# Optimization experiments

Measured on AMD Instinct MI355X. Metric: run time of the kernel, lower is better.

The kernel has to match this reference:

```python
import jax, jax.numpy as jnp
import numpy as np

# Static config (matches init_kwargs)
VOCAB, EMBED, HIDDEN = 32000, 256, 512
SLOTS, MEM_DIM, HEADS, TOPK = 1024, 64, 4, 8
B, T = 16, 128
# beta_read/beta_write are learned scalars but the torch forward detaches them
# via .item(); treat as constants (|beta| + 1e-6 with beta init ~1.0).
BETA_R = 1.0 + 1e-6
BETA_W = 1.0 + 1e-6
EPS = 1e-8


def setup_inputs() -> dict:
    key = jax.random.key(0)
    ks = jax.random.split(key, 16)
    s = 0.02
    HD = HEADS * MEM_DIM
    return {
        "input_seq": jax.random.randint(ks[0], (B, T), 0, VOCAB),
        "E": jax.random.normal(ks[1], (VOCAB, EMBED), jnp.float32) * s,
        "W_ih": jax.random.normal(ks[2], (4 * HIDDEN, EMBED + MEM_DIM), jnp.float32) * s,
        "W_hh": jax.random.normal(ks[3], (4 * HIDDEN, HIDDEN), jnp.float32) * s,
        "b_ih": jnp.zeros((4 * HIDDEN,), jnp.float32),
        "b_hh": jnp.zeros((4 * HIDDEN,), jnp.float32),
        "W_out": jax.random.normal(ks[4], (HIDDEN, VOCAB), jnp.float32) * s,
        "b_out": jnp.zeros((VOCAB,), jnp.float32),
        "W_rk": jax.random.normal(ks[5], (HIDDEN, HD), jnp.float32) * s,
        "b_rk": jnp.zeros((HD,), jnp.float32),
        "W_wk": jax.random.normal(ks[6], (HIDDEN, HD), jnp.float32) * s,
        "b_wk": jnp.zeros((HD,), jnp.float32),
        "W_wv": jax.random.normal(ks[7], (HIDDEN, HD), jnp.float32) * s,
        "b_wv": jnp.zeros((HD,), jnp.float32),
        "W_er": jax.random.normal(ks[8], (HIDDEN, HD), jnp.float32) * s,
        "b_er": jnp.zeros((HD,), jnp.float32),
    }


def _address(memory, keys, beta):
    # memory: [B,S,D], keys: [B,H,D] -> sparse (top-k) content weights [B,H,S]
    mem_n = memory / (jnp.linalg.norm(memory, axis=-1, keepdims=True) + EPS)
    key_n = keys / (jnp.linalg.norm(keys, axis=-1, keepdims=True) + EPS)
    scores = beta * jnp.einsum("bhd,bsd->bhs", key_n, mem_n)
    vals, idx = jax.lax.top_k(scores, TOPK)           # [B,H,K]
    sm = jax.nn.softmax(vals, axis=-1)                # softmax over top-k only
    w = jnp.zeros_like(scores)
    b_ix = jnp.arange(scores.shape[0])[:, None, None]
    h_ix = jnp.arange(HEADS)[None, :, None]
    return w.at[b_ix, h_ix, idx].set(sm)              # [B,H,S]


def reference(input_seq, E, W_ih, W_hh, b_ih, b_hh, W_out, b_out,
              W_rk, b_rk, W_wk, b_wk, W_wv, b_wv, W_er, b_er):
    Bq = input_seq.shape[0]
    memory0 = jnp.full((Bq, SLOTS, MEM_DIM), 1e-6, jnp.float32)
    h0 = jnp.zeros((Bq, HIDDEN), jnp.float32)
    c0 = jnp.zeros((Bq, HIDDEN), jnp.float32)
    r0 = jnp.zeros((Bq, MEM_DIM), jnp.float32)

    def step(carry, x_t):
        memory, h, c, read_vec = carry
        emb = E[x_t]                                          # [B,embed]
        inp = jnp.concatenate([emb, read_vec], axis=-1)
        gates = inp @ W_ih.T + b_ih + h @ W_hh.T + b_hh       # [B,4H]
        i, f, g, o = jnp.split(gates, 4, axis=-1)             # torch LSTM order
        c = jax.nn.sigmoid(f) * c + jax.nn.sigmoid(i) * jnp.tanh(g)
        h = jax.nn.sigmoid(o) * jnp.tanh(c)
        logits = h @ W_out + b_out                            # [B,V]
        rk = (h @ W_rk + b_rk).reshape(Bq, HEADS, MEM_DIM)
        wk = (h @ W_wk + b_wk).reshape(Bq, HEADS, MEM_DIM)
        wv = (h @ W_wv + b_wv).reshape(Bq, HEADS, MEM_DIM)
        er = jax.nn.sigmoid(h @ W_er + b_er).reshape(Bq, HEADS, MEM_DIM)
        # content-addressed top-k read
        rw = _address(memory, rk, BETA_R)                     # [B,H,S]
        read_vec = jnp.einsum("bhs,bsd->bhd", rw, memory).mean(axis=1)
        # erase + add write
        ww = _address(memory, wk, BETA_W)                     # [B,H,S]
        keep = jnp.prod(1.0 - ww[..., None] * er[:, :, None, :], axis=1)
        add = jnp.einsum("bhs,bhd->bsd", ww, wv)
        memory = memory * keep + add
        return (memory, h, c, read_vec), logits

    _, logits_seq = jax.lax.scan(step, (memory0, h0, c0, r0), input_seq.T)
    return jnp.transpose(logits_seq, (1, 0, 2))               # [B,T,V]
```

## Files before the change

### kernel.cpp

```cpp
#include <hip/hip_runtime.h>
#include <hip/hip_bf16.h>
#include <stdint.h>

typedef unsigned int uint;
typedef unsigned long long u64;

#define T_STEPS 128
#define BQ 16
#define HID 512
#define NSLOT 1024
#define MD 64
#define VOCAB 32000
#define NWG 128
#define BETA 1.000001f
#define EPSN 1e-8f

#define L_MEM  0
#define L_NRM  8704
#define L_WS   8832
#define L_HS   12960
#define L_KEY  21216
#define L_KNRM 21728
#define L_SC   21736
#define L_WV   22760
#define L_ER   23016
#define L_WL   23272
#define L_GL   23336
#define L_RV   23592
#define L_TOT  24616

#define AL4(dst, p) asm volatile("global_load_dwordx4 %0, %1, off sc0 sc1" : "=v"(dst) : "v"(p))
#define ALF(dst, p) asm volatile("global_load_dword %0, %1, off sc0 sc1" : "=v"(dst) : "v"(p))
#define AWAIT() do { asm volatile("s_waitcnt vmcnt(0)" ::: "memory"); __builtin_amdgcn_sched_barrier(0); } while(0)

__device__ __forceinline__ float sigm(float x){ return 1.f/(1.f+expf(-x)); }
__device__ __forceinline__ void astoref(float* p, float v){
  __hip_atomic_store(p, v, __ATOMIC_RELAXED, __HIP_MEMORY_SCOPE_AGENT);
}
__device__ __forceinline__ void astoreu64(u64* p, u64 v){
  __hip_atomic_store(p, v, __ATOMIC_RELAXED, __HIP_MEMORY_SCOPE_AGENT);
}
__device__ __forceinline__ u64 aloadu64(const u64* p){
  return __hip_atomic_load((u64*)p, __ATOMIC_RELAXED, __HIP_MEMORY_SCOPE_AGENT);
}
__device__ __forceinline__ uint aloadu32(const uint* p){
  return __hip_atomic_load((uint*)p, __ATOMIC_RELAXED, __HIP_MEMORY_SCOPE_AGENT);
}

__device__ __forceinline__ u64 packsc(float v, int slot){
  uint u = __float_as_uint(v);
  u = (u & 0x80000000u) ? ~u : (u | 0x80000000u);
  return ((u64)u << 10) | (u64)(1023 - slot);
}
__device__ __forceinline__ float unpackval(u64 p){
  uint u = (uint)(p >> 10);
  uint bits = (u & 0x80000000u) ? (u & 0x7fffffffu) : ~u;
  return __uint_as_float(bits);
}
__device__ __forceinline__ int unpackslot(u64 p){ return 1023 - (int)(p & 1023u); }

__device__ __forceinline__ void b_arrive(uint* arrv, uint gen){
  asm volatile("s_waitcnt vmcnt(0)" ::: "memory");
  __syncthreads();
  if (threadIdx.x == 0)
    __hip_atomic_store(arrv + (size_t)blockIdx.x*32, gen, __ATOMIC_RELAXED, __HIP_MEMORY_SCOPE_AGENT);
}
__device__ __forceinline__ void b_wait(uint* arrv, uint gen){
  if (blockIdx.x == 0){
    if (threadIdx.x < NWG){
      while (aloadu32(arrv + (size_t)threadIdx.x*32) < gen)
        __builtin_amdgcn_s_sleep(1);
    }
    __syncthreads();
    if (threadIdx.x < 16)
      __hip_atomic_store(arrv + (size_t)(NWG + threadIdx.x)*32, gen, __ATOMIC_RELAXED, __HIP_MEMORY_SCOPE_AGENT);
    __syncthreads();
  } else {
    if (threadIdx.x == 0){
      while (aloadu32(arrv + (size_t)(NWG + (blockIdx.x & 15))*32) < gen)
        __builtin_amdgcn_s_sleep(1);
    }
    __syncthreads();
  }
}

__global__ __launch_bounds__(256) void prep_emb(const float* __restrict__ E,
                                                const int* __restrict__ seq,
                                                float* __restrict__ EMB){
  int m = blockIdx.x;
  int t = m >> 4, b = m & 15;
  int x = seq[b*T_STEPS + t];
  EMB[(size_t)m*256 + threadIdx.x] = E[(size_t)x*256 + threadIdx.x];
}

__global__ __launch_bounds__(256) void gemm_emb(const float* __restrict__ A,
                                                const float* __restrict__ W_ih,
                                                const float* __restrict__ b_ih,
                                                const float* __restrict__ b_hh,
                                                float* __restrict__ C){
  __shared__ __align__(16) float As[16*68];
  __shared__ __align__(16) float Bs[16*68];
  int mt = blockIdx.x & 31, nt = blockIdx.x >> 5;
  int m0 = mt*64, n0 = nt*64;
  int tx = threadIdx.x & 15, ty = threadIdx.x >> 4;
  float acc[4][4] = {};
  for (int k0 = 0; k0 < 256; k0 += 16){
    int mm = threadIdx.x >> 2, kq = (threadIdx.x & 3)*4;
    float4 a = *(const float4*)(A + (size_t)(m0+mm)*256 + k0 + kq);
    As[(kq+0)*68+mm]=a.x; As[(kq+1)*68+mm]=a.y; As[(kq+2)*68+mm]=a.z; As[(kq+3)*68+mm]=a.w;
    int pp = n0 + mm;
    int r = (pp & 3)*512 + (pp >> 2);
    float4 bv = *(const float4*)(W_ih + (size_t)r*320 + k0 + kq);
    Bs[(kq+0)*68+mm]=bv.x; Bs[(kq+1)*68+mm]=bv.y; Bs[(kq+2)*68+mm]=bv.z; Bs[(kq+3)*68+mm]=bv.w;
    __syncthreads();
    #pragma unroll
    for (int kk = 0; kk < 16; ++kk){
      float4 av = *(const float4*)(As + kk*68 + ty*4);
      float4 bb = *(const float4*)(Bs + kk*68 + tx*4);
      float aa[4] = {av.x,av.y,av.z,av.w};
      float bv2[4] = {bb.x,bb.y,bb.z,bb.w};
      #pragma unroll
      for (int i = 0; i < 4; ++i)
        #pragma unroll
        for (int j = 0; j < 4; ++j)
          acc[i][j] = fmaf(aa[i], bv2[j], acc[i][j]);
    }
    __syncthreads();
  }
  #pragma unroll
  for (int i = 0; i < 4; ++i){
    int m = m0 + ty*4 + i;
    #pragma unroll
    for (int j = 0; j < 4; ++j){
      int pp = n0 + tx*4 + j;
      int r = (pp & 3)*512 + (pp >> 2);
      C[(size_t)m*2048 + pp] = acc[i][j] + b_ih[r] + b_hh[r];
    }
  }
}

__global__ __launch_bounds__(256, 1) void recurrent_kernel(
    const float* __restrict__ W_hh, const float* __restrict__ W_ih,
    const float* __restrict__ W_rk, const float* __restrict__ b_rk,
    const float* __restrict__ W_wk, const float* __restrict__ b_wk,
    const float* __restrict__ W_wv, const float* __restrict__ b_wv,
    const float* __restrict__ W_er, const float* __restrict__ b_er,
    const float* __restrict__ G_emb, float* __restrict__ H_all,
    float* __restrict__ mem_g, float* __restrict__ projbuf,
    float* __restrict__ rv_g, u64* __restrict__ cand,
    u64* __restrict__ wlist, uint* __restrict__ arrv)
{
  __shared__ __align__(16) float smem[L_TOT];
  float* mem_s  = smem + L_MEM;
  float* nrm_s  = smem + L_NRM;
  float* Ws     = smem + L_WS;
  float* hs     = smem + L_HS;
  float* key_s  = smem + L_KEY;
  float* knrm_s = smem + L_KNRM;
  float* sc_s   = smem + L_SC;
  float* wv_s   = smem + L_WV;
  float* er_s   = smem + L_ER;
  u64*   wl_s   = (u64*)(smem + L_WL);
  float* gl     = smem + L_GL;
  float* rv_st  = smem + L_RV;

  const int tid = threadIdx.x;
  const int wg  = blockIdx.x;
  float c_reg = 0.f;

  const int p1_b = tid >> 4, p1_col = tid & 15;
  const int pcol = wg*16 + p1_col;
  const int rrow = (pcol & 3)*512 + (pcol >> 2);
  const int msel = wg >> 5;
  const int col0 = (wg & 31)*8;
  const float* Wm  = (msel==0)? W_rk : (msel==1)? W_wk : (msel==2)? W_wv : W_er;
  const float* bmp = (msel==0)? b_rk : (msel==1)? b_wk : (msel==2)? b_wv : b_er;
  const int bb3 = wg >> 3, rg = wg & 7, s0 = rg*128;
  float* mslice_g = mem_g + ((size_t)bb3*NSLOT + s0)*MD;

  for (int i = tid; i < 8*HID; i += 256){
    int k = i >> 3, j = i & 7;
    Ws[j*516 + k] = Wm[(size_t)k*256 + col0 + j];
  }
  for (int i = tid; i < 128*MD; i += 256){
    mem_s[(i >> 6)*68 + (i & 63)] = 1e-6f;
    astoref(mslice_g + i, 1e-6f);
  }
  gl[p1_b*16 + p1_col] = G_emb[(size_t)p1_b*2048 + pcol];
  __syncthreads();
  if (p1_col < 4){
    float gi = gl[p1_b*16 + p1_col*4 + 0];
    float gf = gl[p1_b*16 + p1_col*4 + 1];
    float gg = gl[p1_b*16 + p1_col*4 + 2];
    float go = gl[p1_b*16 + p1_col*4 + 3];
    c_reg = sigm(gf)*c_reg + sigm(gi)*tanhf(gg);
    float h = sigm(go)*tanhf(c_reg);
    astoref(H_all + (size_t)p1_b*HID + wg*4 + p1_col, h);
  }
  b_arrive(arrv, 1);

  #pragma clang loop unroll(disable)
  for (int t = 0; t < T_STEPS-1; ++t){
    const uint g0 = (uint)(4*t);
    b_wait(arrv, g0 + 1);

    {
      const float4* hsrc = (const float4*)(H_all + (size_t)t*BQ*HID);
      for (int i = tid; i < BQ*HID/4; i += 256){
        int b = i >> 7, q = i & 127;
        *(float4*)(hs + b*516 + q*4) = hsrc[i];
      }
      __syncthreads();
      int b = tid >> 4, o2 = (tid & 15) >> 1, half = tid & 1;
      const float4* wp = (const float4*)(Ws + o2*516 + half*256);
      const float4* xp = (const float4*)(hs + b*516 + half*256);
      float a0 = 0.f, a1 = 0.f;
      #pragma unroll 4
      for (int k = 0; k < 64; k += 2){
        float4 w = wp[k], x = xp[k];
        a0=fmaf(w.x,x.x,a0); a0=fmaf(w.y,x.y,a0); a0=fmaf(w.z,x.z,a0); a0=fmaf(w.w,x.w,a0);
        w = wp[k+1]; x = xp[k+1];
        a1=fmaf(w.x,x.x,a1); a1=fmaf(w.y,x.y,a1); a1=fmaf(w.z,x.z,a1); a1=fmaf(w.w,x.w,a1);
      }
      float acc = a0 + a1;
      float other = __shfl_xor(acc, 1);
      if (half == 0){
        float v = acc + other + bmp[col0 + o2];
        if (msel == 3) v = sigm(v);
        astoref(projbuf + (size_t)(t&1)*BQ*1024 + (size_t)b*1024 + msel*256 + col0 + o2, v);
      }
    }
    b_arrive(arrv, g0 + 2);

    float gp;
    {
      const int parp = (t & 1) ^ 1;
      if (t > 0){
        const float* projp = projbuf + (size_t)parp*BQ*1024 + (size_t)bb3*1024;
        if (tid < 32)
          wl_s[tid] = aloadu64(wlist + (size_t)bb3*32 + tid);
        if (tid < 64){
          float4 v; AL4(v, (const float4*)(projp + 512) + tid); AWAIT();
          *(float4*)(wv_s + tid*4) = v;
        } else if (tid < 128){
          int i = tid - 64;
          float4 v; AL4(v, (const float4*)(projp + 768) + i); AWAIT();
          *(float4*)(er_s + i*4) = v;
        }
      }
      __syncthreads();
      if (t > 0 && tid < 64){
        const int d = tid;
        #pragma unroll 1
        for (int e = 0; e < 32; ++e){
          u64 w64 = wl_s[e];
          int sl = (int)(w64 & 0xffffffffu);
          if (sl >= s0 && sl < s0+128){
            float w = __uint_as_float((uint)(w64 >> 32));
            mem_s[(sl-s0)*68 + d] *= (1.f - w*er_s[(e >> 3)*64 + d]);
          }
        }
        #pragma unroll 1
        for (int e = 0; e < 32; ++e){
          u64 w64 = wl_s[e];
          int sl = (int)(w64 & 0xffffffffu);
          if (sl >= s0 && sl < s0+128){
            float w = __uint_as_float((uint)(w64 >> 32));
            mem_s[(sl-s0)*68 + d] += w*wv_s[(e >> 3)*64 + d];
          }
        }
        #pragma unroll 1
        for (int e = 0; e < 32; ++e){
          u64 w64 = wl_s[e];
          int sl = (int)(w64 & 0xffffffffu);
          if (sl >= s0 && sl < s0+128)
            astoref(mslice_g + (sl-s0)*MD + d, mem_s[(sl-s0)*68 + d]);
        }
      }
      __syncthreads();
      {
        int s = tid >> 1, half = tid & 1;
        const float4* mp = (const float4*)(mem_s + s*68 + half*32);
        float sum = 0.f;
        #pragma unroll
        for (int q = 0; q < 8; ++q){
          float4 v = mp[q];
          sum = fmaf(v.x,v.x,sum); sum = fmaf(v.y,v.y,sum);
          sum = fmaf(v.z,v.z,sum); sum = fmaf(v.w,v.w,sum);
        }
        sum += __shfl_xor(sum, 1);
        if (half == 0) nrm_s[s] = sqrtf(sum) + EPSN;
      }
      {
        float a0 = G_emb[(size_t)((t+1)*BQ + p1_b)*2048 + pcol];
        float a1 = 0.f, a2 = 0.f, a3 = 0.f;
        const float4* wh = (const float4*)(W_hh + (size_t)rrow*HID);
        const float4* xv = (const float4*)(hs + p1_b*516);
        #pragma unroll 2
        for (int k = 0; k < 128; k += 4){
          float4 w, x;
          w=wh[k+0]; x=xv[k+0]; a0=fmaf(w.x,x.x,a0); a0=fmaf(w.y,x.y,a0); a0=fmaf(w.z,x.z,a0); a0=fmaf(w.w,x.w,a0);
          w=wh[k+1]; x=xv[k+1]; a1=fmaf(w.x,x.x,a1); a1=fmaf(w.y,x.y,a1); a1=fmaf(w.z,x.z,a1); a1=fmaf(w.w,x.w,a1);
          w=wh[k+2]; x=xv[k+2]; a2=fmaf(w.x,x.x,a2); a2=fmaf(w.y,x.y,a2); a2=fmaf(w.z,x.z,a2); a2=fmaf(w.w,x.w,a2);
          w=wh[k+3]; x=xv[k+3]; a3=fmaf(w.x,x.x,a3); a3=fmaf(w.y,x.y,a3); a3=fmaf(w.w,x.w,a3); a3=fmaf(w.z,x.z,a3);
        }
        gp = (a0+a1)+(a2+a3);
      }
    }
    b_wait(arrv, g0 + 2);

    {
      const float* projb = projbuf + (size_t)(t&1)*BQ*1024 + (size_t)bb3*1024;
      if (tid < 128){
        float4 kv; AL4(kv, (const float4*)projb + tid); AWAIT();
        *(float4*)(key_s + tid*4) = kv;
      }
      __syncthreads();
      if (tid < 8){
        const float4* kp = (const float4*)(key_s + tid*MD);
        float sum = 0.f;
        #pragma unroll
        for (int q = 0; q < 16; ++q){
          float4 v = kp[q];
          sum = fmaf(v.x,v.x,sum); sum = fmaf(v.y,v.y,sum);
          sum = fmaf(v.z,v.z,sum); sum = fmaf(v.w,v.w,sum);
        }
        knrm_s[tid] = sqrtf(sum) + EPSN;
      }
      __syncthreads();
      {
        int s = tid >> 1, kh = tid & 1;
        const float4* mp = (const float4*)(mem_s + s*68);
        float rnm = 1.f / nrm_s[s];
        float acc4[4] = {0.f,0.f,0.f,0.f};
        #pragma unroll
        for (int q = 0; q < 16; ++q){
          float4 m = mp[q];
          #pragma unroll
          for (int kk = 0; kk < 4; ++kk){
            float4 k4 = *(const float4*)(key_s + (kh*4+kk)*MD + q*4);
            acc4[kk] = fmaf(m.x,k4.x,acc4[kk]); acc4[kk] = fmaf(m.y,k4.y,acc4[kk]);
            acc4[kk] = fmaf(m.z,k4.z,acc4[kk]); acc4[kk] = fmaf(m.w,k4.w,acc4[kk]);
          }
        }
        #pragma unroll
        for (int kk = 0; kk < 4; ++kk){
          int key = kh*4 + kk;
          sc_s[key*128 + s] = BETA * acc4[kk] * rnm / knrm_s[key];
        }
      }
      __syncthreads();
      {
        int wid = tid >> 6, lane = tid & 63;
        #pragma unroll
        for (int kk = 0; kk < 2; ++kk){
          int key = wid*2 + kk;
          u64 p0 = packsc(sc_s[key*128 + lane],      s0 + lane);
          u64 p1 = packsc(sc_s[key*128 + 64 + lane], s0 + 64 + lane);
          #pragma unroll
          for (int r = 0; r < 8; ++r){
            u64 m = p0 > p1 ? p0 : p1;
            #pragma unroll
            for (int o = 32; o; o >>= 1){ u64 q = __shfl_xor(m, o); if (q > m) m = q; }
            if (p0 == m) p0 = 0; else if (p1 == m) p1 = 0;
            if (lane == 0) astoreu64(cand + (((size_t)bb3*8 + key)*8 + rg)*8 + r, m);
          }
        }
      }
    }
    b_arrive(arrv, g0 + 3);
    b_wait(arrv, g0 + 3);

    if (wg < BQ){
      const int bb = wg;
      int wid = tid >> 6, lane = tid & 63;
      #pragma unroll
      for (int kk = 0; kk < 2; ++kk){
        int key = wid*2 + kk;
        u64 pv = aloadu64(cand + (((size_t)bb*8 + key)*8 + (lane >> 3))*8 + (lane & 7));
        u64 sel = 0;
        #pragma unroll
        for (int r = 0; r < 8; ++r){
          u64 m = pv;
          #pragma unroll
          for (int o = 32; o; o >>= 1){ u64 q = __shfl_xor(m, o); if (q > m) m = q; }
          if (pv == m) pv = 0;
          if (lane == r) sel = m;
        }
        float val = unpackval(sel);
        int slot = unpackslot(sel);
        float vmax = __shfl(val, 0);
        float e = (lane < 8) ? expf(val - vmax) : 0.f;
        float ssum = e;
        #pragma unroll
        for (int o = 32; o; o >>= 1) ssum += __shfl_xor(ssum, o);
        float w = e / ssum;
        if (key < 4){
          int sls[8];
          #pragma unroll
          for (int i = 0; i < 8; ++i) sls[i] = __shfl(slot, i);
          float mv[8];
          #pragma unroll
          for (int i = 0; i < 8; ++i)
            ALF(mv[i], mem_g + ((size_t)bb*NSLOT + sls[i])*MD + lane);
          AWAIT();
          float acc = 0.f;
          #pragma unroll
          for (int i = 0; i < 8; ++i) acc = fmaf(__shfl(w, i), mv[i], acc);
          rv_st[key*64 + lane] = acc;
        } else if (lane < 8){
          astoreu64(wlist + (size_t)bb*32 + (key-4)*8 + lane,
                    ((u64)__float_as_uint(w) << 32) | (u64)(uint)slot);
        }
      }
      __syncthreads();
      if (tid < 64){
        float m = 0.25f*(rv_st[tid] + rv_st[64+tid] + rv_st[128+tid] + rv_st[192+tid]);
        astoref(rv_g + (size_t)bb*MD + tid, m);
      }
    }
    b_arrive(arrv, g0 + 4);
    b_wait(arrv, g0 + 4);

    {
      float4 rvv; AL4(rvv, (const float4*)rv_g + tid); AWAIT();
      *(float4*)(rv_st + tid*4) = rvv;
      __syncthreads();
      float a0 = gp, a1 = 0.f;
      const float4* wi = (const float4*)(W_ih + (size_t)rrow*320 + 256);
      const float4* xr = (const float4*)(rv_st + p1_b*64);
      #pragma unroll
      for (int k = 0; k < 16; k += 2){
        float4 w = wi[k], x = xr[k];
        a0=fmaf(w.x,x.x,a0); a0=fmaf(w.y,x.y,a0); a0=fmaf(w.z,x.z,a0); a0=fmaf(w.w,x.w,a0);
        w = wi[k+1]; x = xr[k+1];
        a1=fmaf(w.x,x.x,a1); a1=fmaf(w.y,x.y,a1); a1=fmaf(w.z,x.z,a1); a1=fmaf(w.w,x.w,a1);
      }
      gl[p1_b*16 + p1_col] = a0 + a1;
      __syncthreads();
      if (p1_col < 4){
        float gi = gl[p1_b*16 + p1_col*4 + 0];
        float gf = gl[p1_b*16 + p1_col*4 + 1];
        float gg = gl[p1_b*16 + p1_col*4 + 2];
        float go = gl[p1_b*16 + p1_col*4 + 3];
        c_reg = sigm(gf)*c_reg + sigm(gi)*tanhf(gg);
        float h = sigm(go)*tanhf(c_reg);
        astoref(H_all + (size_t)((t+1)*BQ + p1_b)*HID + wg*4 + p1_col, h);
      }
    }
    b_arrive(arrv, g0 + 5);
  }
}

__global__ __launch_bounds__(256) void gemm_out(const float* __restrict__ A,
                                                const float* __restrict__ Bmat,
                                                const float* __restrict__ bias,
                                                float* __restrict__ C){
  __shared__ __align__(16) float As[16*132];
  __shared__ __align__(16) float Bs[16*64];
  int mt = blockIdx.x & 15, nt = blockIdx.x >> 4;
  int m0 = mt*128, n0 = nt*64;
  int tx = threadIdx.x & 15, ty = threadIdx.x >> 4;
  float acc[8][4] = {};
  for (int k0 = 0; k0 < 512; k0 += 16){
    int mm = threadIdx.x >> 1, kq = (threadIdx.x & 1)*8;
    float4 a0 = *(const float4*)(A + (size_t)(m0+mm)*512 + k0 + kq);
    float4 a1 = *(const float4*)(A + (size_t)(m0+mm)*512 + k0 + kq + 4);
    As[(kq+0)*132+mm]=a0.x; As[(kq+1)*132+mm]=a0.y; As[(kq+2)*132+mm]=a0.z; As[(kq+3)*132+mm]=a0.w;
    As[(kq+4)*132+mm]=a1.x; As[(kq+5)*132+mm]=a1.y; As[(kq+6)*132+mm]=a1.z; As[(kq+7)*132+mm]=a1.w;
    int kk2 = threadIdx.x >> 4, nq = (threadIdx.x & 15)*4;
    *(float4*)(Bs + kk2*64 + nq) = *(const float4*)(Bmat + (size_t)(k0+kk2)*VOCAB + n0 + nq);
    __syncthreads();
    #pragma unroll
    for (int kk = 0; kk < 16; ++kk){
      float4 x0 = *(const float4*)(As + kk*132 + ty*8);
      float4 x1 = *(const float4*)(As + kk*132 + ty*8 + 4);
      float4 bv = *(const float4*)(Bs + kk*64 + tx*4);
      float aa[8] = {x0.x,x0.y,x0.z,x0.w,x1.x,x1.y,x1.z,x1.w};
      float bb[4] = {bv.x,bv.y,bv.z,bv.w};
      #pragma unroll
      for (int i = 0; i < 8; ++i)
        #pragma unroll
        for (int j = 0; j < 4; ++j)
          acc[i][j] = fmaf(aa[i], bb[j], acc[i][j]);
    }
    __syncthreads();
  }
  #pragma unroll
  for (int i = 0; i < 8; ++i){
    int m = m0 + ty*8 + i;
    int bq = m & 15, tt = m >> 4;
    float* crow = C + ((size_t)bq*T_STEPS + tt)*VOCAB + n0 + tx*4;
    #pragma unroll
    for (int j = 0; j < 4; ++j) crow[j] = acc[i][j] + bias[n0 + tx*4 + j];
  }
}

extern "C" void kernel_launch(void* const* d_in, const int* in_sizes, int n_in,
                              void* d_out, int out_size, void* d_ws, size_t ws_size,
                              hipStream_t stream){
  const int*   seq   = (const int*)d_in[0];
  const float* E     = (const float*)d_in[1];
  const float* W_ih  = (const float*)d_in[2];
  const float* W_hh  = (const float*)d_in[3];
  const float* b_ih  = (const float*)d_in[4];
  const float* b_hh  = (const float*)d_in[5];
  const float* W_out = (const float*)d_in[6];
  const float* b_out = (const float*)d_in[7];
  const float* W_rk  = (const float*)d_in[8];
  const float* b_rk  = (const float*)d_in[9];
  const float* W_wk  = (const float*)d_in[10];
  const float* b_wk  = (const float*)d_in[11];
  const float* W_wv  = (const float*)d_in[12];
  const float* b_wv  = (const float*)d_in[13];
  const float* W_er  = (const float*)d_in[14];
  const float* b_er  = (const float*)d_in[15];
  float* out = (float*)d_out;
  (void)in_sizes; (void)n_in; (void)out_size; (void)ws_size;

  char* ws = (char*)d_ws;
  size_t off = 0;
  auto alloc = [&](size_t bytes) -> void* {
    off = (off + 255) & ~(size_t)255;
    void* p = ws + off;
    off += bytes;
    return p;
  };
  float* EMB     = (float*)alloc((size_t)2048*256*4);
  float* G_emb   = (float*)alloc((size_t)2048*2048*4);
  float* H_all   = (float*)alloc((size_t)2048*512*4);
  float* memb    = (float*)alloc((size_t)16*1024*64*4);
  float* projbuf = (float*)alloc((size_t)2*16*1024*4);
  float* rv_g    = (float*)alloc((size_t)16*64*4);
  u64*   cand    = (u64*)alloc((size_t)16*8*8*8*8);
  u64*   wlist   = (u64*)alloc((size_t)16*32*8);
  uint*  arrv    = (uint*)alloc((size_t)(NWG+16)*32*4);

  hipMemsetAsync(arrv, 0, (size_t)(NWG+16)*32*4, stream);
  prep_emb<<<2048, 256, 0, stream>>>(E, seq, EMB);
  gemm_emb<<<1024, 256, 0, stream>>>(EMB, W_ih, b_ih, b_hh, G_emb);
  recurrent_kernel<<<NWG, 256, 0, stream>>>(W_hh, W_ih, W_rk, b_rk, W_wk, b_wk,
                                            W_wv, b_wv, W_er, b_er,
                                            G_emb, H_all, memb, projbuf, rv_g,
                                            cand, wlist, arrv);
  gemm_out<<<16*500, 256, 0, stream>>>(H_all, W_out, b_out, out);
}
```

Measured before the change: 7.368 ms.

## Replace global barriers with point-to-point flags and dedicated per-batch LSTM workgroups

Replaces the centralized grid barrier (workgroup 0 gathers arrivals and rebroadcasts) with fine-grained per-producer flag lines that consumers poll directly. Adds 16 dedicated workgroups, one per batch row, that run top-k selection, the read vector and the LSTM cell update, while 128 workers handle memory slices, projections (now done by only 32 workgroups reading weights from global) and partial gate dot products. The read-vector part of W_ih is pre-transposed into a smem-resident tile. The goal is to cut barrier latency on the serial critical path per timestep, at the cost of more polling traffic and a more complex dependency chain.

```diff
diff --git a/kernel.cpp b/kernel.cpp
--- a/kernel.cpp
+++ b/kernel.cpp
@@ -11,32 +11,31 @@
 #define NSLOT 1024
 #define MD 64
 #define VOCAB 32000
-#define NWG 128
 #define BETA 1.000001f
 #define EPSN 1e-8f
 
-#define L_MEM  0
-#define L_NRM  8704
-#define L_WS   8832
-#define L_HS   12960
-#define L_KEY  21216
-#define L_KNRM 21728
-#define L_SC   21736
-#define L_WV   22760
-#define L_ER   23016
-#define L_WL   23272
-#define L_GL   23336
-#define L_RV   23592
-#define L_TOT  24616
+#define NWK 128
+#define NBT 16
+
+#define LF_FH(b)  ((b)*32)
+#define LF_FP(w)  ((16+(w))*32)
+#define LF_FC(w)  ((48+(w))*32)
+#define LF_FRV(b) ((176+(b))*32)
+#define LF_FG(w)  ((192+(w))*32)
+#define NLINES    320
 
 #define AL4(dst, p) asm volatile("global_load_dwordx4 %0, %1, off sc0 sc1" : "=v"(dst) : "v"(p))
 #define ALF(dst, p) asm volatile("global_load_dword %0, %1, off sc0 sc1" : "=v"(dst) : "v"(p))
 #define AWAIT() do { asm volatile("s_waitcnt vmcnt(0)" ::: "memory"); __builtin_amdgcn_sched_barrier(0); } while(0)
+#define DRAIN() asm volatile("s_waitcnt vmcnt(0)" ::: "memory")
 
 __device__ __forceinline__ float sigm(float x){ return 1.f/(1.f+expf(-x)); }
 __device__ __forceinline__ void astoref(float* p, float v){
   __hip_atomic_store(p, v, __ATOMIC_RELAXED, __HIP_MEMORY_SCOPE_AGENT);
 }
+__device__ __forceinline__ void astoreu32(uint* p, uint v){
+  __hip_atomic_store(p, v, __ATOMIC_RELAXED, __HIP_MEMORY_SCOPE_AGENT);
+}
 __device__ __forceinline__ void astoreu64(u64* p, u64 v){
   __hip_atomic_store(p, v, __ATOMIC_RELAXED, __HIP_MEMORY_SCOPE_AGENT);
 }
@@ -45,6 +44,9 @@
 }
 __device__ __forceinline__ uint aloadu32(const uint* p){
   return __hip_atomic_load((uint*)p, __ATOMIC_RELAXED, __HIP_MEMORY_SCOPE_AGENT);
+}
+__device__ __forceinline__ void poll1(const uint* p, uint gen){
+  while (aloadu32(p) < gen) __builtin_amdgcn_s_sleep(2);
 }
 
 __device__ __forceinline__ u64 packsc(float v, int slot){
@@ -59,36 +61,23 @@
 }
 __device__ __forceinline__ int unpackslot(u64 p){ return 1023 - (int)(p & 1023u); }
 
-__device__ __forceinline__ void b_arrive(uint* arrv, uint gen){
-  asm volatile("s_waitcnt vmcnt(0)" ::: "memory");
-  __syncthreads();
-  if (threadIdx.x == 0)
-    __hip_atomic_store(arrv + (size_t)blockIdx.x*32, gen, __ATOMIC_RELAXED, __HIP_MEMORY_SCOPE_AGENT);
-}
-__device__ __forceinline__ void b_wait(uint* arrv, uint gen){
-  if (blockIdx.x == 0){
-    if (threadIdx.x < NWG){
-      while (aloadu32(arrv + (size_t)threadIdx.x*32) < gen)
-        __builtin_amdgcn_s_sleep(1);
-    }
-    __syncthreads();
-    if (threadIdx.x < 16)
-      __hip_atomic_store(arrv + (size_t)(NWG + threadIdx.x)*32, gen, __ATOMIC_RELAXED, __HIP_MEMORY_SCOPE_AGENT);
-    __syncthreads();
-  } else {
-    if (threadIdx.x == 0){
-      while (aloadu32(arrv + (size_t)(NWG + (blockIdx.x & 15))*32) < gen)
-        __builtin_amdgcn_s_sleep(1);
-    }
-    __syncthreads();
-  }
-}
+#define L_MEM  0
+#define L_NRM  8704
+#define L_HS   8832
+#define L_KEY  17088
+#define L_KNRM 17600
+#define L_SC   17608
+#define L_WV   18632
+#define L_ER   18888
+#define L_WL   19144
+#define L_RVS  19208
+#define L_WTS  20232
+#define L_TOT  21256
 
 __global__ __launch_bounds__(256) void prep_emb(const float* __restrict__ E,
                                                 const int* __restrict__ seq,
                                                 float* __restrict__ EMB){
-  int m = blockIdx.x;
-  int t = m >> 4, b = m & 15;
+  int m = blockIdx.x, t = m >> 4, b = m & 15;
   int x = seq[b*T_STEPS + t];
   EMB[(size_t)m*256 + threadIdx.x] = E[(size_t)x*256 + threadIdx.x];
 }
@@ -139,180 +128,187 @@
   }
 }
 
-__global__ __launch_bounds__(256, 1) void recurrent_kernel(
-    const float* __restrict__ W_hh, const float* __restrict__ W_ih,
+__global__ __launch_bounds__(256) void make_wrvT(const float* __restrict__ W_ih,
+                                                 float* __restrict__ WT){
+  int idx = blockIdx.x*256 + threadIdx.x;
+  int k = idx >> 11, p = idx & 2047;
+  int r = (p & 3)*512 + (p >> 2);
+  WT[idx] = W_ih[(size_t)r*320 + 256 + k];
+}
+
+__global__ __launch_bounds__(256) void recur_kernel(
+    const float* __restrict__ W_hh, const float* __restrict__ WT,
     const float* __restrict__ W_rk, const float* __restrict__ b_rk,
     const float* __restrict__ W_wk, const float* __restrict__ b_wk,
     const float* __restrict__ W_wv, const float* __restrict__ b_wv,
     const float* __restrict__ W_er, const float* __restrict__ b_er,
     const float* __restrict__ G_emb, float* __restrict__ H_all,
-    float* __restrict__ mem_g, float* __restrict__ projbuf,
-    float* __restrict__ rv_g, u64* __restrict__ cand,
+    float* __restrict__ H_pub, float* __restrict__ mem_g,
+    float* __restrict__ projpub, float* __restrict__ gatespub,
+    float* __restrict__ rvpub, u64* __restrict__ cand,
     u64* __restrict__ wlist, uint* __restrict__ arrv)
 {
   __shared__ __align__(16) float smem[L_TOT];
-  float* mem_s  = smem + L_MEM;
-  float* nrm_s  = smem + L_NRM;
-  float* Ws     = smem + L_WS;
-  float* hs     = smem + L_HS;
-  float* key_s  = smem + L_KEY;
-  float* knrm_s = smem + L_KNRM;
-  float* sc_s   = smem + L_SC;
-  float* wv_s   = smem + L_WV;
-  float* er_s   = smem + L_ER;
-  u64*   wl_s   = (u64*)(smem + L_WL);
-  float* gl     = smem + L_GL;
-  float* rv_st  = smem + L_RV;
-
   const int tid = threadIdx.x;
   const int wg  = blockIdx.x;
-  float c_reg = 0.f;
-
-  const int p1_b = tid >> 4, p1_col = tid & 15;
-  const int pcol = wg*16 + p1_col;
-  const int rrow = (pcol & 3)*512 + (pcol >> 2);
-  const int msel = wg >> 5;
-  const int col0 = (wg & 31)*8;
-  const float* Wm  = (msel==0)? W_rk : (msel==1)? W_wk : (msel==2)? W_wv : W_er;
-  const float* bmp = (msel==0)? b_rk : (msel==1)? b_wk : (msel==2)? b_wv : b_er;
-  const int bb3 = wg >> 3, rg = wg & 7, s0 = rg*128;
-  float* mslice_g = mem_g + ((size_t)bb3*NSLOT + s0)*MD;
-
-  for (int i = tid; i < 8*HID; i += 256){
-    int k = i >> 3, j = i & 7;
-    Ws[j*516 + k] = Wm[(size_t)k*256 + col0 + j];
-  }
-  for (int i = tid; i < 128*MD; i += 256){
-    mem_s[(i >> 6)*68 + (i & 63)] = 1e-6f;
-    astoref(mslice_g + i, 1e-6f);
-  }
-  gl[p1_b*16 + p1_col] = G_emb[(size_t)p1_b*2048 + pcol];
-  __syncthreads();
-  if (p1_col < 4){
-    float gi = gl[p1_b*16 + p1_col*4 + 0];
-    float gf = gl[p1_b*16 + p1_col*4 + 1];
-    float gg = gl[p1_b*16 + p1_col*4 + 2];
-    float go = gl[p1_b*16 + p1_col*4 + 3];
-    c_reg = sigm(gf)*c_reg + sigm(gi)*tanhf(gg);
-    float h = sigm(go)*tanhf(c_reg);
-    astoref(H_all + (size_t)p1_b*HID + wg*4 + p1_col, h);
-  }
-  b_arrive(arrv, 1);
-
-  #pragma clang loop unroll(disable)
-  for (int t = 0; t < T_STEPS-1; ++t){
-    const uint g0 = (uint)(4*t);
-    b_wait(arrv, g0 + 1);
-
+
+  if (wg < NWK){
+    float* mem_s  = smem + L_MEM;
+    float* nrm_s  = smem + L_NRM;
+    float* hs     = smem + L_HS;
+    float* key_s  = smem + L_KEY;
+    float* knrm_s = smem + L_KNRM;
+    float* sc_s   = smem + L_SC;
+    float* wv_s   = smem + L_WV;
+    float* er_s   = smem + L_ER;
+    u64*   wl_s   = (u64*)(smem + L_WL);
+    float* rv_s   = smem + L_RVS;
+    float* WT_s   = smem + L_WTS;
+
+    const int b_s = wg >> 3, rg = wg & 7, s0 = rg*128;
+    const int gb = tid >> 4, gc = tid & 15;
+    const int pcol = wg*16 + gc;
+    const int rrow = (pcol & 3)*512 + (pcol >> 2);
+    float* mslice_g = mem_g + ((size_t)b_s*NSLOT + s0)*MD;
+    const float* W1 = (wg < 16) ? W_rk : W_wk;
+    const float* B1 = (wg < 16) ? b_rk : b_wk;
+    const float* W2 = (wg < 16) ? W_wv : W_er;
+    const float* B2 = (wg < 16) ? b_wv : b_er;
+    const int cc = (wg & 15)*16 + gc;
+    const float pb1 = (wg < 32) ? B1[cc] : 0.f;
+    const float pb2 = (wg < 32) ? B2[cc] : 0.f;
+
+    for (int i = tid; i < 64*16; i += 256){
+      int d = i >> 4, c = i & 15;
+      WT_s[i] = WT[(size_t)d*2048 + wg*16 + c];
+    }
+    for (int i = tid; i < 128*MD; i += 256){
+      mem_s[(i >> 6)*68 + (i & 63)] = 1e-6f;
+      astoref(mslice_g + i, 1e-6f);
+    }
+    __syncthreads();
     {
-      const float4* hsrc = (const float4*)(H_all + (size_t)t*BQ*HID);
-      for (int i = tid; i < BQ*HID/4; i += 256){
-        int b = i >> 7, q = i & 127;
-        *(float4*)(hs + b*516 + q*4) = hsrc[i];
-      }
-      __syncthreads();
-      int b = tid >> 4, o2 = (tid & 15) >> 1, half = tid & 1;
-      const float4* wp = (const float4*)(Ws + o2*516 + half*256);
-      const float4* xp = (const float4*)(hs + b*516 + half*256);
-      float a0 = 0.f, a1 = 0.f;
-      #pragma unroll 4
-      for (int k = 0; k < 64; k += 2){
-        float4 w = wp[k], x = xp[k];
-        a0=fmaf(w.x,x.x,a0); a0=fmaf(w.y,x.y,a0); a0=fmaf(w.z,x.z,a0); a0=fmaf(w.w,x.w,a0);
-        w = wp[k+1]; x = xp[k+1];
-        a1=fmaf(w.x,x.x,a1); a1=fmaf(w.y,x.y,a1); a1=fmaf(w.z,x.z,a1); a1=fmaf(w.w,x.w,a1);
-      }
-      float acc = a0 + a1;
-      float other = __shfl_xor(acc, 1);
-      if (half == 0){
-        float v = acc + other + bmp[col0 + o2];
-        if (msel == 3) v = sigm(v);
-        astoref(projbuf + (size_t)(t&1)*BQ*1024 + (size_t)b*1024 + msel*256 + col0 + o2, v);
-      }
-    }
-    b_arrive(arrv, g0 + 2);
-
-    float gp;
-    {
-      const int parp = (t & 1) ^ 1;
+      int s = tid >> 1, half = tid & 1;
+      const float4* mp = (const float4*)(mem_s + s*68 + half*32);
+      float sum = 0.f;
+      #pragma unroll
+      for (int q = 0; q < 8; ++q){
+        float4 v = mp[q];
+        sum = fmaf(v.x,v.x,sum); sum = fmaf(v.y,v.y,sum);
+        sum = fmaf(v.z,v.z,sum); sum = fmaf(v.w,v.w,sum);
+      }
+      sum += __shfl_xor(sum, 1);
+      if (half == 0) nrm_s[s] = sqrtf(sum) + EPSN;
+    }
+    __syncthreads();
+
+    #pragma clang loop unroll(disable)
+    for (int t = 0; t < T_STEPS-1; ++t){
+      const int par = t & 1, parp = par ^ 1;
       if (t > 0){
-        const float* projp = projbuf + (size_t)parp*BQ*1024 + (size_t)bb3*1024;
-        if (tid < 32)
-          wl_s[tid] = aloadu64(wlist + (size_t)bb3*32 + tid);
+        if (tid < 32) wl_s[tid] = aloadu64(wlist + (size_t)b_s*32 + tid);
         if (tid < 64){
-          float4 v; AL4(v, (const float4*)(projp + 512) + tid); AWAIT();
+          float4 v; AL4(v, (const float4*)(projpub + (size_t)parp*BQ*1024 + (size_t)b_s*1024 + 512) + tid);
+          AWAIT();
           *(float4*)(wv_s + tid*4) = v;
         } else if (tid < 128){
           int i = tid - 64;
-          float4 v; AL4(v, (const float4*)(projp + 768) + i); AWAIT();
+          float4 v; AL4(v, (const float4*)(projpub + (size_t)parp*BQ*1024 + (size_t)b_s*1024 + 768) + i);
+          AWAIT();
           *(float4*)(er_s + i*4) = v;
         }
-      }
-      __syncthreads();
-      if (t > 0 && tid < 64){
-        const int d = tid;
-        #pragma unroll 1
-        for (int e = 0; e < 32; ++e){
-          u64 w64 = wl_s[e];
-          int sl = (int)(w64 & 0xffffffffu);
-          if (sl >= s0 && sl < s0+128){
-            float w = __uint_as_float((uint)(w64 >> 32));
-            mem_s[(sl-s0)*68 + d] *= (1.f - w*er_s[(e >> 3)*64 + d]);
-          }
-        }
-        #pragma unroll 1
-        for (int e = 0; e < 32; ++e){
-          u64 w64 = wl_s[e];
-          int sl = (int)(w64 & 0xffffffffu);
-          if (sl >= s0 && sl < s0+128){
-            float w = __uint_as_float((uint)(w64 >> 32));
-            mem_s[(sl-s0)*68 + d] += w*wv_s[(e >> 3)*64 + d];
-          }
-        }
-        #pragma unroll 1
-        for (int e = 0; e < 32; ++e){
-          u64 w64 = wl_s[e];
-          int sl = (int)(w64 & 0xffffffffu);
-          if (sl >= s0 && sl < s0+128)
-            astoref(mslice_g + (sl-s0)*MD + d, mem_s[(sl-s0)*68 + d]);
-        }
-      }
-      __syncthreads();
-      {
-        int s = tid >> 1, half = tid & 1;
-        const float4* mp = (const float4*)(mem_s + s*68 + half*32);
-        float sum = 0.f;
-        #pragma unroll
-        for (int q = 0; q < 8; ++q){
-          float4 v = mp[q];
-          sum = fmaf(v.x,v.x,sum); sum = fmaf(v.y,v.y,sum);
-          sum = fmaf(v.z,v.z,sum); sum = fmaf(v.w,v.w,sum);
-        }
-        sum += __shfl_xor(sum, 1);
-        if (half == 0) nrm_s[s] = sqrtf(sum) + EPSN;
-      }
-      {
-        float a0 = G_emb[(size_t)((t+1)*BQ + p1_b)*2048 + pcol];
-        float a1 = 0.f, a2 = 0.f, a3 = 0.f;
-        const float4* wh = (const float4*)(W_hh + (size_t)rrow*HID);
-        const float4* xv = (const float4*)(hs + p1_b*516);
-        #pragma unroll 2
-        for (int k = 0; k < 128; k += 4){
-          float4 w, x;
-          w=wh[k+0]; x=xv[k+0]; a0=fmaf(w.x,x.x,a0); a0=fmaf(w.y,x.y,a0); a0=fmaf(w.z,x.z,a0); a0=fmaf(w.w,x.w,a0);
-          w=wh[k+1]; x=xv[k+1]; a1=fmaf(w.x,x.x,a1); a1=fmaf(w.y,x.y,a1); a1=fmaf(w.z,x.z,a1); a1=fmaf(w.w,x.w,a1);
-          w=wh[k+2]; x=xv[k+2]; a2=fmaf(w.x,x.x,a2); a2=fmaf(w.y,x.y,a2); a2=fmaf(w.z,x.z,a2); a2=fmaf(w.w,x.w,a2);
-          w=wh[k+3]; x=xv[k+3]; a3=fmaf(w.x,x.x,a3); a3=fmaf(w.y,x.y,a3); a3=fmaf(w.w,x.w,a3); a3=fmaf(w.z,x.z,a3);
-        }
-        gp = (a0+a1)+(a2+a3);
-      }
-    }
-    b_wait(arrv, g0 + 2);
-
-    {
-      const float* projb = projbuf + (size_t)(t&1)*BQ*1024 + (size_t)bb3*1024;
+        __syncthreads();
+        if (tid < 64){
+          const int d = tid;
+          #pragma unroll 1
+          for (int e = 0; e < 32; ++e){
+            u64 w64 = wl_s[e];
+            int sl = (int)(w64 & 0xffffffffu);
+            if (sl >= s0 && sl < s0+128){
+              float w = __uint_as_float((uint)(w64 >> 32));
+              mem_s[(sl-s0)*68 + d] *= (1.f - w*er_s[(e >> 3)*64 + d]);
+            }
+          }
+          #pragma unroll 1
+          for (int e = 0; e < 32; ++e){
+            u64 w64 = wl_s[e];
+            int sl = (int)(w64 & 0xffffffffu);
+            if (sl >= s0 && sl < s0+128){
+              float w = __uint_as_float((uint)(w64 >> 32));
+              mem_s[(sl-s0)*68 + d] += w*wv_s[(e >> 3)*64 + d];
+            }
+          }
+          #pragma unroll 1
+          for (int e = 0; e < 32; ++e){
+            u64 w64 = wl_s[e];
+            int sl = (int)(w64 & 0xffffffffu);
+            if (sl >= s0 && sl < s0+128)
+              astoref(mslice_g + (sl-s0)*MD + d, mem_s[(sl-s0)*68 + d]);
+          }
+        }
+        __syncthreads();
+        {
+          int s = tid >> 1, half = tid & 1;
+          const float4* mp = (const float4*)(mem_s + s*68 + half*32);
+          float sum = 0.f;
+          #pragma unroll
+          for (int q = 0; q < 8; ++q){
+            float4 v = mp[q];
+            sum = fmaf(v.x,v.x,sum); sum = fmaf(v.y,v.y,sum);
+            sum = fmaf(v.z,v.z,sum); sum = fmaf(v.w,v.w,sum);
+          }
+          sum += __shfl_xor(sum, 1);
+          if (half == 0) nrm_s[s] = sqrtf(sum) + EPSN;
+        }
+      }
+      if (tid < 16) poll1(arrv + LF_FH(tid), (uint)(t+1));
+      __syncthreads();
+      {
+        float4 v0,v1,v2,v3,v4,v5,v6,v7;
+        const float4* hp = (const float4*)H_pub;
+        AL4(v0, hp + tid);        AL4(v1, hp + tid + 256);
+        AL4(v2, hp + tid + 512);  AL4(v3, hp + tid + 768);
+        AL4(v4, hp + tid + 1024); AL4(v5, hp + tid + 1280);
+        AL4(v6, hp + tid + 1536); AL4(v7, hp + tid + 1792);
+        AWAIT();
+        int i;
+        i = tid;        *(float4*)(hs + (i>>7)*516 + (i&127)*4) = v0;
+        i = tid + 256;  *(float4*)(hs + (i>>7)*516 + (i&127)*4) = v1;
+        i = tid + 512;  *(float4*)(hs + (i>>7)*516 + (i&127)*4) = v2;
+        i = tid + 768;  *(float4*)(hs + (i>>7)*516 + (i&127)*4) = v3;
+        i = tid + 1024; *(float4*)(hs + (i>>7)*516 + (i&127)*4) = v4;
+        i = tid + 1280; *(float4*)(hs + (i>>7)*516 + (i&127)*4) = v5;
+        i = tid + 1536; *(float4*)(hs + (i>>7)*516 + (i&127)*4) = v6;
+        i = tid + 1792; *(float4*)(hs + (i>>7)*516 + (i&127)*4) = v7;
+      }
+      __syncthreads();
+      if (wg < 32){
+        float a0=0.f,a1=0.f,b0=0.f,b1=0.f;
+        const float* hp = hs + gb*516;
+        const float* w1 = W1 + cc;
+        const float* w2 = W2 + cc;
+        #pragma unroll 4
+        for (int k = 0; k < 512; k += 2){
+          float h0 = hp[k], h1 = hp[k+1];
+          a0 = fmaf(h0, w1[(size_t)k*256], a0);
+          b0 = fmaf(h0, w2[(size_t)k*256], b0);
+          a1 = fmaf(h1, w1[(size_t)(k+1)*256], a1);
+          b1 = fmaf(h1, w2[(size_t)(k+1)*256], b1);
+        }
+        float v1 = a0 + a1 + pb1;
+        float v2 = b0 + b1 + pb2;
+        if (wg >= 16) v2 = sigm(v2);
+        astoref(projpub + (size_t)par*BQ*1024 + (size_t)gb*1024 + wg*16 + gc, v1);
+        astoref(projpub + (size_t)par*BQ*1024 + (size_t)gb*1024 + 512 + wg*16 + gc, v2);
+      }
+      DRAIN();
+      __syncthreads();
+      if (wg < 32 && tid == 0) astoreu32(arrv + LF_FP(wg), (uint)(t+1));
+      if (tid < 32) poll1(arrv + LF_FP(tid), (uint)(t+1));
+      __syncthreads();
       if (tid < 128){
-        float4 kv; AL4(kv, (const float4*)projb + tid); AWAIT();
+        float4 kv; AL4(kv, (const float4*)(projpub + (size_t)par*BQ*1024 + (size_t)b_s*1024) + tid);
+        AWAIT();
         *(float4*)(key_s + tid*4) = kv;
       }
       __syncthreads();
@@ -363,92 +359,141 @@
             #pragma unroll
             for (int o = 32; o; o >>= 1){ u64 q = __shfl_xor(m, o); if (q > m) m = q; }
             if (p0 == m) p0 = 0; else if (p1 == m) p1 = 0;
-            if (lane == 0) astoreu64(cand + (((size_t)bb3*8 + key)*8 + rg)*8 + r, m);
-          }
-        }
-      }
-    }
-    b_arrive(arrv, g0 + 3);
-    b_wait(arrv, g0 + 3);
-
-    if (wg < BQ){
-      const int bb = wg;
-      int wid = tid >> 6, lane = tid & 63;
-      #pragma unroll
-      for (int kk = 0; kk < 2; ++kk){
-        int key = wid*2 + kk;
-        u64 pv = aloadu64(cand + (((size_t)bb*8 + key)*8 + (lane >> 3))*8 + (lane & 7));
-        u64 sel = 0;
-        #pragma unroll
-        for (int r = 0; r < 8; ++r){
-          u64 m = pv;
+            if (lane == 0) astoreu64(cand + (((size_t)b_s*8 + key)*8 + rg)*8 + r, m);
+          }
+        }
+      }
+      DRAIN();
+      __syncthreads();
+      if (tid == 0) astoreu32(arrv + LF_FC(wg), (uint)(t+1));
+      float gpv;
+      {
+        float a0 = G_emb[(size_t)((t+1)*BQ + gb)*2048 + pcol];
+        float a1 = 0.f, a2 = 0.f, a3 = 0.f;
+        const float4* wh = (const float4*)(W_hh + (size_t)rrow*HID);
+        const float4* xv = (const float4*)(hs + gb*516);
+        #pragma unroll 2
+        for (int k = 0; k < 128; k += 4){
+          float4 w, x;
+          w=wh[k+0]; x=xv[k+0]; a0=fmaf(w.x,x.x,a0); a0=fmaf(w.y,x.y,a0); a0=fmaf(w.z,x.z,a0); a0=fmaf(w.w,x.w,a0);
+          w=wh[k+1]; x=xv[k+1]; a1=fmaf(w.x,x.x,a1); a1=fmaf(w.y,x.y,a1); a1=fmaf(w.z,x.z,a1); a1=fmaf(w.w,x.w,a1);
+          w=wh[k+2]; x=xv[k+2]; a2=fmaf(w.x,x.x,a2); a2=fmaf(w.y,x.y,a2); a2=fmaf(w.z,x.z,a2); a2=fmaf(w.w,x.w,a2);
+          w=wh[k+3]; x=xv[k+3]; a3=fmaf(w.x,x.x,a3); a3=fmaf(w.y,x.y,a3); a3=fmaf(w.z,x.z,a3); a3=fmaf(w.w,x.w,a3);
+        }
+        gpv = (a0+a1)+(a2+a3);
+      }
+      if (tid < 16) poll1(arrv + LF_FRV(tid), (uint)(t+1));
+      __syncthreads();
+      {
+        float4 v; AL4(v, (const float4*)rvpub + tid); AWAIT();
+        *(float4*)(rv_s + tid*4) = v;
+      }
+      __syncthreads();
+      {
+        float acc = gpv;
+        #pragma unroll 8
+        for (int d = 0; d < 64; ++d)
+          acc = fmaf(rv_s[gb*64 + d], WT_s[d*16 + gc], acc);
+        astoref(gatespub + (size_t)gb*2048 + pcol, acc);
+      }
+      DRAIN();
+      __syncthreads();
+      if (tid == 0) astoreu32(arrv + LF_FG(wg), (uint)(t+1));
+    }
+  } else {
+    const int b = wg - NWK;
+    float* rv_st = smem;
+    float c0, c1;
+    {
+      float4 gA = *(const float4*)(G_emb + (size_t)b*2048 + tid*8);
+      float4 gB = *(const float4*)(G_emb + (size_t)b*2048 + tid*8 + 4);
+      c0 = sigm(gA.x)*tanhf(gA.z);
+      float h0v = sigm(gA.w)*tanhf(c0);
+      c1 = sigm(gB.x)*tanhf(gB.z);
+      float h1v = sigm(gB.w)*tanhf(c1);
+      astoref(H_pub + (size_t)b*HID + tid*2,     h0v);
+      astoref(H_pub + (size_t)b*HID + tid*2 + 1, h1v);
+      H_all[(size_t)b*HID + tid*2]     = h0v;
+      H_all[(size_t)b*HID + tid*2 + 1] = h1v;
+    }
+    DRAIN();
+    __syncthreads();
+    if (tid == 0) astoreu32(arrv + LF_FH(b), 1u);
+
+    #pragma clang loop unroll(disable)
+    for (int t = 0; t < T_STEPS-1; ++t){
+      if (tid < 8) poll1(arrv + LF_FC(b*8 + tid), (uint)(t+1));
+      __syncthreads();
+      {
+        int wid = tid >> 6, lane = tid & 63;
+        #pragma unroll
+        for (int kk = 0; kk < 2; ++kk){
+          int key = wid*2 + kk;
+          u64 pv = aloadu64(cand + (((size_t)b*8 + key)*8 + (lane >> 3))*8 + (lane & 7));
+          u64 sel = 0;
           #pragma unroll
-          for (int o = 32; o; o >>= 1){ u64 q = __shfl_xor(m, o); if (q > m) m = q; }
-          if (pv == m) pv = 0;
-          if (lane == r) sel = m;
-        }
-        float val = unpackval(sel);
-        int slot = unpackslot(sel);
-        float vmax = __shfl(val, 0);
-        float e = (lane < 8) ? expf(val - vmax) : 0.f;
-        float ssum = e;
-        #pragma unroll
-        for (int o = 32; o; o >>= 1) ssum += __shfl_xor(ssum, o);
-        float w = e / ssum;
-        if (key < 4){
-          int sls[8];
+          for (int r = 0; r < 8; ++r){
+            u64 m = pv;
+            #pragma unroll
+            for (int o = 32; o; o >>= 1){ u64 q = __shfl_xor(m, o); if (q > m) m = q; }
+            if (pv == m) pv = 0;
+            if (lane == r) sel = m;
+          }
+          float val = unpackval(sel);
+          int slot = unpackslot(sel);
+          float vmax = __shfl(val, 0);
+          float e = (lane < 8) ? expf(val - vmax) : 0.f;
+          float ssum = e;
           #pragma unroll
-          for (int i = 0; i < 8; ++i) sls[i] = __shfl(slot, i);
-          float mv[8];
-          #pragma unroll
-          for (int i = 0; i < 8; ++i)
-            ALF(mv[i], mem_g + ((size_t)bb*NSLOT + sls[i])*MD + lane);
-          AWAIT();
-          float acc = 0.f;
-          #pragma unroll
-          for (int i = 0; i < 8; ++i) acc = fmaf(__shfl(w, i), mv[i], acc);
-          rv_st[key*64 + lane] = acc;
-        } else if (lane < 8){
-          astoreu64(wlist + (size_t)bb*32 + (key-4)*8 + lane,
-                    ((u64)__float_as_uint(w) << 32) | (u64)(uint)slot);
+          for (int o = 32; o; o >>= 1) ssum += __shfl_xor(ssum, o);
+          float w = e / ssum;
+          if (key < 4){
+            int sls[8];
+            #pragma unroll
+            for (int i = 0; i < 8; ++i) sls[i] = __shfl(slot, i);
+            float mv[8];
+            #pragma unroll
+            for (int i = 0; i < 8; ++i)
+              ALF(mv[i], mem_g + ((size_t)b*NSLOT + sls[i])*MD + lane);
+            AWAIT();
+            float acc = 0.f;
+            #pragma unroll
+            for (int i = 0; i < 8; ++i) acc = fmaf(__shfl(w, i), mv[i], acc);
+            rv_st[key*64 + lane] = acc;
+          } else if (lane < 8){
+            astoreu64(wlist + (size_t)b*32 + (key-4)*8 + lane,
+                      ((u64)__float_as_uint(w) << 32) | (u64)(uint)slot);
+          }
         }
       }
       __syncthreads();
       if (tid < 64){
         float m = 0.25f*(rv_st[tid] + rv_st[64+tid] + rv_st[128+tid] + rv_st[192+tid]);
-        astoref(rv_g + (size_t)bb*MD + tid, m);
-      }
-    }
-    b_arrive(arrv, g0 + 4);
-    b_wait(arrv, g0 + 4);
-
-    {
-      float4 rvv; AL4(rvv, (const float4*)rv_g + tid); AWAIT();
-      *(float4*)(rv_st + tid*4) = rvv;
-      __syncthreads();
-      float a0 = gp, a1 = 0.f;
-      const float4* wi = (const float4*)(W_ih + (size_t)rrow*320 + 256);
-      const float4* xr = (const float4*)(rv_st + p1_b*64);
-      #pragma unroll
-      for (int k = 0; k < 16; k += 2){
-        float4 w = wi[k], x = xr[k];
-        a0=fmaf(w.x,x.x,a0); a0=fmaf(w.y,x.y,a0); a0=fmaf(w.z,x.z,a0); a0=fmaf(w.w,x.w,a0);
-        w = wi[k+1]; x = xr[k+1];
-        a1=fmaf(w.x,x.x,a1); a1=fmaf(w.y,x.y,a1); a1=fmaf(w.z,x.z,a1); a1=fmaf(w.w,x.w,a1);
-      }
-      gl[p1_b*16 + p1_col] = a0 + a1;
-      __syncthreads();
-      if (p1_col < 4){
-        float gi = gl[p1_b*16 + p1_col*4 + 0];
-        float gf = gl[p1_b*16 + p1_col*4 + 1];
-        float gg = gl[p1_b*16 + p1_col*4 + 2];
-        float go = gl[p1_b*16 + p1_col*4 + 3];
-        c_reg = sigm(gf)*c_reg + sigm(gi)*tanhf(gg);
-        float h = sigm(go)*tanhf(c_reg);
-        astoref(H_all + (size_t)((t+1)*BQ + p1_b)*HID + wg*4 + p1_col, h);
-      }
-    }
-    b_arrive(arrv, g0 + 5);
+        astoref(rvpub + (size_t)b*MD + tid, m);
+      }
+      DRAIN();
+      __syncthreads();
+      if (tid == 0) astoreu32(arrv + LF_FRV(b), (uint)(t+1));
+      if (tid < 128) poll1(arrv + LF_FG(tid), (uint)(t+1));
+      __syncthreads();
+      {
+        float4 gA, gB;
+        AL4(gA, (const float4*)(gatespub + (size_t)b*2048) + tid*2);
+        AL4(gB, (const float4*)(gatespub + (size_t)b*2048) + tid*2 + 1);
+        AWAIT();
+        c0 = sigm(gA.y)*c0 + sigm(gA.x)*tanhf(gA.z);
+        float h0v = sigm(gA.w)*tanhf(c0);
+        c1 = sigm(gB.y)*c1 + sigm(gB.x)*tanhf(gB.z);
+        float h1v = sigm(gB.w)*tanhf(c1);
+        astoref(H_pub + (size_t)b*HID + tid*2,     h0v);
+        astoref(H_pub + (size_t)b*HID + tid*2 + 1, h1v);
+        H_all[(size_t)((t+1)*BQ + b)*HID + tid*2]     = h0v;
+        H_all[(size_t)((t+1)*BQ + b)*HID + tid*2 + 1] = h1v;
+      }
+      DRAIN();
+      __syncthreads();
+      if (tid == 0) astoreu32(arrv + LF_FH(b), (uint)(t+2));
+    }
   }
 }
 
@@ -526,22 +571,25 @@
     off += bytes;
     return p;
   };
-  float* EMB     = (float*)alloc((size_t)2048*256*4);
-  float* G_emb   = (float*)alloc((size_t)2048*2048*4);
-  float* H_all   = (float*)alloc((size_t)2048*512*4);
-  float* memb    = (float*)alloc((size_t)16*1024*64*4);
-  float* projbuf = (float*)alloc((size_t)2*16*1024*4);
-  float* rv_g    = (float*)alloc((size_t)16*64*4);
-  u64*   cand    = (u64*)alloc((size_t)16*8*8*8*8);
-  u64*   wlist   = (u64*)alloc((size_t)16*32*8);
-  uint*  arrv    = (uint*)alloc((size_t)(NWG+16)*32*4);
-
-  hipMemsetAsync(arrv, 0, (size_t)(NWG+16)*32*4, stream);
+  float* EMB      = (float*)alloc((size_t)2048*256*4);
+  float* G_emb    = (float*)alloc((size_t)2048*2048*4);
+  float* H_all    = (float*)alloc((size_t)2048*512*4);
+  float* H_pub    = (float*)alloc((size_t)16*512*4);
+  float* mem_g    = (float*)alloc((size_t)16*1024*64*4);
+  float* projpub  = (float*)alloc((size_t)2*16*1024*4);
+  float* gatespub = (float*)alloc((size_t)16*2048*4);
+  float* rvpub    = (float*)alloc((size_t)16*64*4);
+  u64*   cand     = (u64*)alloc((size_t)16*8*8*8*8);
+  u64*   wlist    = (u64*)alloc((size_t)16*32*8);
+  float* WT       = (float*)alloc((size_t)64*2048*4);
+  uint*  arrv     = (uint*)alloc((size_t)NLINES*32*4);
+
+  hipMemsetAsync(arrv, 0, (size_t)NLINES*32*4, stream);
   prep_emb<<<2048, 256, 0, stream>>>(E, seq, EMB);
   gemm_emb<<<1024, 256, 0, stream>>>(EMB, W_ih, b_ih, b_hh, G_emb);
-  recurrent_kernel<<<NWG, 256, 0, stream>>>(W_hh, W_ih, W_rk, b_rk, W_wk, b_wk,
-                                            W_wv, b_wv, W_er, b_er,
-                                            G_emb, H_all, memb, projbuf, rv_g,
-                                            cand, wlist, arrv);
+  make_wrvT<<<512, 256, 0, stream>>>(W_ih, WT);
+  recur_kernel<<<NWK + NBT, 256, 0, stream>>>(
+      W_hh, WT, W_rk, b_rk, W_wk, b_wk, W_wv, b_wv, W_er, b_er,
+      G_emb, H_all, H_pub, mem_g, projpub, gatespub, rvpub, cand, wlist, arrv);
   gemm_out<<<16*500, 256, 0, stream>>>(H_all, W_out, b_out, out);
 }
```

After: 7.006 ms. 4.9% less time.
